# Kernel optimization log

Hardware: AMD Instinct MI355X
Metric: run time of the kernel (lower is better)

The kernel has to match this reference:

```python
import jax, jax.numpy as jnp
import numpy as np

B, N, F = 4, 3000, 128

def setup_inputs() -> dict:
    key = jax.random.key(0)
    k1, k2, k3, k4 = jax.random.split(key, 4)
    x = jax.random.normal(k1, (B, N, F), dtype=jnp.float32)
    adj = jax.random.uniform(k2, (B, N, N), dtype=jnp.float32)
    h0 = jax.random.normal(k3, (B, N, F), dtype=jnp.float32)
    stdv = 1.0 / np.sqrt(F)
    theta = jax.random.uniform(k4, (F, F), dtype=jnp.float32, minval=-stdv, maxval=stdv)
    return {
        "x": x, "adj": adj, "h0": h0, "theta": theta,
        "lamda": jnp.float32(0.5), "alpha": jnp.float32(0.1), "l": 4,
    }

def _normalize_adj(adj):
    # add self loops, then D^{-1/2} A D^{-1/2} via elementwise row/col scaling
    # (same math as diag-embed + inverse + two bmms in the original)
    n = adj.shape[1]
    adj = adj + jnp.eye(n, dtype=adj.dtype)
    deg = jnp.sum(adj, axis=2)                      # [B, N]
    d_inv_sqrt = jax.lax.rsqrt(deg)                 # [B, N]
    return d_inv_sqrt[:, :, None] * adj * d_inv_sqrt[:, None, :]

def reference(x, adj, h0, theta, lamda, alpha, l):
    adj_n = _normalize_adj(adj)
    beta = jnp.log(lamda / l + 1.0)
    hi = jnp.einsum('bnm,bmf->bnf', adj_n, x)       # aggregation
    support = (1.0 - alpha) * hi + alpha * h0       # variant=False path
    r = support
    out = beta * jnp.einsum('bnf,fg->bng', support, theta) + (1.0 - beta) * r
    return out
```

## Files before the change

kernel.cpp:

```cpp
#include <hip/hip_runtime.h>
#include <hip/hip_bf16.h>
#include <math.h>

#define BB 4
#define NN 3000
#define NR 3008
#define NC 3072
#define FF 128
#define NKC 96
#define NIT 188
#define TS  532

typedef __bf16 bf16x8 __attribute__((ext_vector_type(8)));
typedef __bf16 bf16x4 __attribute__((ext_vector_type(4)));
typedef __bf16 bf16x8a __attribute__((ext_vector_type(8), aligned(8)));
typedef __bf16 bf16x4a __attribute__((ext_vector_type(4), aligned(4)));
typedef float  f32x4  __attribute__((ext_vector_type(4)));

__global__ __launch_bounds__(256) void k_degpk2(const float* __restrict__ adj,
                                                float* __restrict__ dis,
                                                __bf16* __restrict__ apk) {
    int wid  = (blockIdx.x * 256 + threadIdx.x) >> 6;
    int lane = threadIdx.x & 63;
    if (wid >= BB * NR) return;
    int b = wid / NR, i = wid - b * NR;
    const bool rowv = i < NN;
    const float4* row4 = (const float4*)(adj + ((size_t)b * NN + i) * NN);
    __bf16* prow = apk + ((size_t)b * NR + i) * NC;
    float s = 0.f;
    for (int c = lane; c < 768; c += 64) {
        float4 v = {0.f, 0.f, 0.f, 0.f};
        if (rowv && c < 750) v = row4[c];
        s += (v.x + v.y) + (v.z + v.w);
        bf16x4a o;
        o[0] = (__bf16)v.x; o[1] = (__bf16)v.y;
        o[2] = (__bf16)v.z; o[3] = (__bf16)v.w;
        *(bf16x4a*)(prow + c * 4) = o;
    }
    for (int off = 32; off > 0; off >>= 1) s += __shfl_down(s, off, 64);
    if (lane == 0 && rowv) dis[b * NN + i] = 1.0f / sqrtf(s + 1.0f);
}

__global__ __launch_bounds__(256) void k_xpk(const float* __restrict__ x,
                                             const float* __restrict__ dis,
                                             const float* __restrict__ theta,
                                             __bf16* __restrict__ xpk,
                                             __bf16* __restrict__ thpk) {
    int b  = blockIdx.y, kc = blockIdx.x;
    int t  = threadIdx.x, w = t >> 6, l = t & 63;
    int m  = l & 15, q = l >> 4;
    #pragma unroll
    for (int h = 0; h < 2; ++h) {
        int nt = w + h * 4;
        int f  = nt * 16 + m;
        bf16x8 v;
        #pragma unroll
        for (int j = 0; j < 8; ++j) {
            int k = kc * 32 + q * 8 + j;
            float val = 0.f;
            if (k < NN) val = dis[b * NN + k] * x[((size_t)b * NN + k) * FF + f];
            v[j] = (__bf16)val;
        }
        *(bf16x8*)(xpk + ((size_t)(b * 8 + nt) * NKC + kc) * 512 + l * 8) = v;
    }
    if (b == 0 && kc < 4) {
        #pragma unroll
        for (int h = 0; h < 2; ++h) {
            int nt = w + h * 4;
            bf16x8 v;
            #pragma unroll
            for (int j = 0; j < 8; ++j) {
                int k = kc * 32 + q * 8 + j;
                v[j] = (__bf16)theta[k * FF + nt * 16 + m];
            }
            *(bf16x8*)(thpk + ((size_t)(nt * 4 + kc)) * 512 + l * 8) = v;
        }
    }
}

__global__ __launch_bounds__(256) void k_agg3(const __bf16* __restrict__ apk,
                                              const __bf16* __restrict__ xpk,
                                              const __bf16* __restrict__ thpk,
                                              const float* __restrict__ x,
                                              const float* __restrict__ h0,
                                              const float* __restrict__ dis,
                                              float* __restrict__ out,
                                              const float* __restrict__ alpha_p,
                                              const float* __restrict__ lamda_p,
                                              const int* __restrict__ l_p) {
    __shared__ __bf16 tile[2][16][TS];
    __shared__ __bf16 stile[16][140];
    const int id = blockIdx.x;
    const int b  = (id >> 1) & 3;
    const int it = (id >> 3) * 2 + (id & 1);
    const int i0 = it * 16;
    const int t  = threadIdx.x, w = t >> 6, l = t & 63;
    const int m  = l & 15, quad = l >> 4;
    const int n0 = w * 32;
    const __bf16* Abase = apk + ((size_t)b * NR + i0) * NC;
    const __bf16* B0 = xpk + ((size_t)(b * 8 + 2 * w) * NKC) * 512 + l * 8;
    const __bf16* B1 = B0 + (size_t)NKC * 512;
    f32x4 acc0 = {0.f, 0.f, 0.f, 0.f};
    f32x4 acc1 = {0.f, 0.f, 0.f, 0.f};

    bf16x8a st[4];
    auto load_chunk = [&](int c) {
        #pragma unroll
        for (int i = 0; i < 4; ++i) {
            int row = i * 4 + w;
            st[i] = *(const bf16x8a*)(Abase + (size_t)row * NC + c * 512 + l * 8);
        }
    };
    auto store_chunk = [&](int cb) {
        #pragma unroll
        for (int i = 0; i < 4; ++i) {
            int row = i * 4 + w;
            *(bf16x8a*)&tile[cb][row][l * 8] = st[i];
        }
    };

    load_chunk(0);
    store_chunk(0);
    __syncthreads();
    for (int c = 0; c < 6; ++c) {
        int cb = c & 1;
        if (c < 5) load_chunk(c + 1);
        #pragma unroll 4
        for (int kcl = 0; kcl < 16; ++kcl) {
            int kc = c * 16 + kcl;
            bf16x8 a = *(const bf16x8a*)&tile[cb][m][kcl * 32 + quad * 8];
            bf16x8 b0 = *(const bf16x8*)(B0 + (size_t)kc * 512);
            bf16x8 b1 = *(const bf16x8*)(B1 + (size_t)kc * 512);
            acc0 = __builtin_amdgcn_mfma_f32_16x16x32_bf16(a, b0, acc0, 0, 0, 0);
            acc1 = __builtin_amdgcn_mfma_f32_16x16x32_bf16(a, b1, acc1, 0, 0, 0);
        }
        if (c < 5) store_chunk(cb ^ 1);
        __syncthreads();
    }

    const float alpha = *alpha_p;
    const float beta  = logf(*lamda_p / (float)(*l_p) + 1.0f);
    float s0v[4], s1v[4];
    #pragma unroll
    for (int r = 0; r < 4; ++r) {
        int row  = quad * 4 + r;
        int irow = i0 + row;
        float s0 = 0.f, s1 = 0.f;
        if (irow < NN) {
            float  di   = dis[b * NN + irow];
            size_t base = ((size_t)b * NN + irow) * FF;
            int c0 = n0 + m, c1 = n0 + 16 + m;
            s0 = (1.f - alpha) * (di * acc0[r] + di * di * x[base + c0]) + alpha * h0[base + c0];
            s1 = (1.f - alpha) * (di * acc1[r] + di * di * x[base + c1]) + alpha * h0[base + c1];
        }
        s0v[r] = s0; s1v[r] = s1;
        stile[row][n0 + m]      = (__bf16)s0;
        stile[row][n0 + 16 + m] = (__bf16)s1;
    }
    __syncthreads();
    f32x4 o0 = {0.f, 0.f, 0.f, 0.f};
    f32x4 o1 = {0.f, 0.f, 0.f, 0.f};
    const __bf16* T0 = thpk + (size_t)(2 * w * 4) * 512 + l * 8;
    const __bf16* T1 = T0 + 4 * 512;
    #pragma unroll
    for (int kc = 0; kc < 4; ++kc) {
        bf16x4a alo = *(const bf16x4a*)&stile[m][kc * 32 + quad * 8];
        bf16x4a ahi = *(const bf16x4a*)&stile[m][kc * 32 + quad * 8 + 4];
        bf16x8 a = __builtin_shufflevector(alo, ahi, 0, 1, 2, 3, 4, 5, 6, 7);
        bf16x8 tb0 = *(const bf16x8*)(T0 + (size_t)kc * 512);
        bf16x8 tb1 = *(const bf16x8*)(T1 + (size_t)kc * 512);
        o0 = __builtin_amdgcn_mfma_f32_16x16x32_bf16(a, tb0, o0, 0, 0, 0);
        o1 = __builtin_amdgcn_mfma_f32_16x16x32_bf16(a, tb1, o1, 0, 0, 0);
    }
    const float omb = 1.f - beta;
    #pragma unroll
    for (int r = 0; r < 4; ++r) {
        int irow = i0 + quad * 4 + r;
        if (irow < NN) {
            size_t base = ((size_t)b * NN + irow) * FF;
            out[base + n0 + m]      = beta * o0[r] + omb * s0v[r];
            out[base + n0 + 16 + m] = beta * o1[r] + omb * s1v[r];
        }
    }
}

__global__ __launch_bounds__(256) void k_deg(const float* __restrict__ adj,
                                             float* __restrict__ dis) {
    int wid  = (blockIdx.x * 256 + threadIdx.x) >> 6;
    int lane = threadIdx.x & 63;
    if (wid >= BB * NN) return;
    const float4* row = (const float4*)(adj + (size_t)wid * NN);
    float s = 0.f;
    for (int c = lane; c < NN / 4; c += 64) {
        float4 v = row[c];
        s += (v.x + v.y) + (v.z + v.w);
    }
    for (int off = 32; off > 0; off >>= 1) s += __shfl_down(s, off, 64);
    if (lane == 0) dis[wid] = 1.0f / sqrtf(s + 1.0f);
}

__global__ __launch_bounds__(256) void k_agg(const float* __restrict__ adj,
                                             const __bf16* __restrict__ xpk,
                                             const __bf16* __restrict__ thpk,
                                             const float* __restrict__ x,
                                             const float* __restrict__ h0,
                                             const float* __restrict__ dis,
                                             float* __restrict__ out,
                                             const float* __restrict__ alpha_p,
                                             const float* __restrict__ lamda_p,
                                             const int* __restrict__ l_p) {
    __shared__ __bf16 tile[2][16][TS];
    __shared__ __bf16 stile[16][140];
    const int id = blockIdx.x;
    const int b  = (id >> 1) & 3;
    const int it = (id >> 3) * 2 + (id & 1);
    const int i0 = it * 16;
    const int t  = threadIdx.x, w = t >> 6, l = t & 63;
    const int m  = l & 15, quad = l >> 4;
    const int n0 = w * 32;
    const __bf16* B0 = xpk + ((size_t)(b * 8 + 2 * w) * NKC) * 512 + l * 8;
    const __bf16* B1 = B0 + (size_t)NKC * 512;
    f32x4 acc0 = {0.f, 0.f, 0.f, 0.f};
    f32x4 acc1 = {0.f, 0.f, 0.f, 0.f};

    float4 pu[4], pv[4];
    auto load_chunk = [&](int c) {
        #pragma unroll
        for (int i = 0; i < 4; ++i) {
            int row  = i * 4 + w;
            int irow = i0 + row;
            int col  = c * 512 + l * 8;
            float4 u = {0.f, 0.f, 0.f, 0.f}, v = {0.f, 0.f, 0.f, 0.f};
            if (irow < NN && col < NN) {
                const float* p = adj + ((size_t)b * NN + irow) * NN + col;
                u = *(const float4*)p;
                v = *(const float4*)(p + 4);
            }
            pu[i] = u; pv[i] = v;
        }
    };
    auto store_chunk = [&](int cb) {
        #pragma unroll
        for (int i = 0; i < 4; ++i) {
            int row = i * 4 + w;
            bf16x8a s;
            s[0] = (__bf16)pu[i].x; s[1] = (__bf16)pu[i].y;
            s[2] = (__bf16)pu[i].z; s[3] = (__bf16)pu[i].w;
            s[4] = (__bf16)pv[i].x; s[5] = (__bf16)pv[i].y;
            s[6] = (__bf16)pv[i].z; s[7] = (__bf16)pv[i].w;
            *(bf16x8a*)&tile[cb][row][l * 8] = s;
        }
    };

    load_chunk(0);
    store_chunk(0);
    __syncthreads();
    for (int c = 0; c < 6; ++c) {
        int cb = c & 1;
        if (c < 5) load_chunk(c + 1);
        #pragma unroll 4
        for (int kcl = 0; kcl < 16; ++kcl) {
            int kc = c * 16 + kcl;
            bf16x8 a = *(const bf16x8a*)&tile[cb][m][kcl * 32 + quad * 8];
            bf16x8 b0 = *(const bf16x8*)(B0 + (size_t)kc * 512);
            bf16x8 b1 = *(const bf16x8*)(B1 + (size_t)kc * 512);
            acc0 = __builtin_amdgcn_mfma_f32_16x16x32_bf16(a, b0, acc0, 0, 0, 0);
            acc1 = __builtin_amdgcn_mfma_f32_16x16x32_bf16(a, b1, acc1, 0, 0, 0);
        }
        if (c < 5) store_chunk(cb ^ 1);
        __syncthreads();
    }

    const float alpha = *alpha_p;
    const float beta  = logf(*lamda_p / (float)(*l_p) + 1.0f);
    float s0v[4], s1v[4];
    #pragma unroll
    for (int r = 0; r < 4; ++r) {
        int row  = quad * 4 + r;
        int irow = i0 + row;
        float s0 = 0.f, s1 = 0.f;
        if (irow < NN) {
            float  di   = dis[b * NN + irow];
            size_t base = ((size_t)b * NN + irow) * FF;
            int c0 = n0 + m, c1 = n0 + 16 + m;
            s0 = (1.f - alpha) * (di * acc0[r] + di * di * x[base + c0]) + alpha * h0[base + c0];
            s1 = (1.f - alpha) * (di * acc1[r] + di * di * x[base + c1]) + alpha * h0[base + c1];
        }
        s0v[r] = s0; s1v[r] = s1;
        stile[row][n0 + m]      = (__bf16)s0;
        stile[row][n0 + 16 + m] = (__bf16)s1;
    }
    __syncthreads();
    f32x4 o0 = {0.f, 0.f, 0.f, 0.f};
    f32x4 o1 = {0.f, 0.f, 0.f, 0.f};
    const __bf16* T0 = thpk + (size_t)(2 * w * 4) * 512 + l * 8;
    const __bf16* T1 = T0 + 4 * 512;
    #pragma unroll
    for (int kc = 0; kc < 4; ++kc) {
        bf16x4a alo = *(const bf16x4a*)&stile[m][kc * 32 + quad * 8];
        bf16x4a ahi = *(const bf16x4a*)&stile[m][kc * 32 + quad * 8 + 4];
        bf16x8 a = __builtin_shufflevector(alo, ahi, 0, 1, 2, 3, 4, 5, 6, 7);
        bf16x8 tb0 = *(const bf16x8*)(T0 + (size_t)kc * 512);
        bf16x8 tb1 = *(const bf16x8*)(T1 + (size_t)kc * 512);
        o0 = __builtin_amdgcn_mfma_f32_16x16x32_bf16(a, tb0, o0, 0, 0, 0);
        o1 = __builtin_amdgcn_mfma_f32_16x16x32_bf16(a, tb1, o1, 0, 0, 0);
    }
    const float omb = 1.f - beta;
    #pragma unroll
    for (int r = 0; r < 4; ++r) {
        int irow = i0 + quad * 4 + r;
        if (irow < NN) {
            size_t base = ((size_t)b * NN + irow) * FF;
            out[base + n0 + m]      = beta * o0[r] + omb * s0v[r];
            out[base + n0 + 16 + m] = beta * o1[r] + omb * s1v[r];
        }
    }
}

__global__ __launch_bounds__(256) void k_thpk_fb(const float* __restrict__ theta,
                                                 __bf16* __restrict__ thpk) {
    int kc = blockIdx.x;
    int t  = threadIdx.x, w = t >> 6, l = t & 63;
    int m  = l & 15, q = l >> 4;
    #pragma unroll
    for (int h = 0; h < 2; ++h) {
        int nt = w + h * 4;
        bf16x8 v;
        #pragma unroll
        for (int j = 0; j < 8; ++j) {
            int k = kc * 32 + q * 8 + j;
            v[j] = (__bf16)theta[k * FF + nt * 16 + m];
        }
        *(bf16x8*)(thpk + ((size_t)(nt * 4 + kc)) * 512 + l * 8) = v;
    }
}

__global__ __launch_bounds__(256) void k_xpk_fb(const float* __restrict__ x,
                                                const float* __restrict__ dis,
                                                __bf16* __restrict__ xpk) {
    int b  = blockIdx.y, kc = blockIdx.x;
    int t  = threadIdx.x, w = t >> 6, l = t & 63;
    int m  = l & 15, q = l >> 4;
    #pragma unroll
    for (int h = 0; h < 2; ++h) {
        int nt = w + h * 4;
        int f  = nt * 16 + m;
        bf16x8 v;
        #pragma unroll
        for (int j = 0; j < 8; ++j) {
            int k = kc * 32 + q * 8 + j;
            float val = 0.f;
            if (k < NN) val = dis[b * NN + k] * x[((size_t)b * NN + k) * FF + f];
            v[j] = (__bf16)val;
        }
        *(bf16x8*)(xpk + ((size_t)(b * 8 + nt) * NKC + kc) * 512 + l * 8) = v;
    }
}


extern "C" void kernel_launch(void* const* d_in, const int* in_sizes, int n_in,
                              void* d_out, int out_size, void* d_ws, size_t ws_size,
                              hipStream_t stream) {
    const float* x      = (const float*)d_in[0];
    const float* adj    = (const float*)d_in[1];
    const float* h0     = (const float*)d_in[2];
    const float* theta  = (const float*)d_in[3];
    const float* lamda  = (const float*)d_in[4];
    const float* alpha  = (const float*)d_in[5];
    const int*   l      = (const int*)d_in[6];
    float* out = (float*)d_out;

    char* ws = (char*)d_ws;

    const size_t APK_OFF = 3276800;
    const size_t WS_NEED = APK_OFF + (size_t)BB * NR * NC * 2;

    if (ws_size >= WS_NEED) {
        float*  dis  = (float*)ws;
        __bf16* thpk = (__bf16*)(ws + 65536);
        __bf16* xpk  = (__bf16*)(ws + 131072);
        __bf16* apk  = (__bf16*)(ws + APK_OFF);

        k_degpk2<<<dim3((BB * NR) / 4), 256, 0, stream>>>(adj, dis, apk);
        k_xpk<<<dim3(NKC, BB), 256, 0, stream>>>(x, dis, theta, xpk, thpk);
        k_agg3<<<dim3(NIT * BB), 256, 0, stream>>>(apk, xpk, thpk, x, h0, dis, out,
                                                   alpha, lamda, l);
    } else {
        float*  dis  = (float*)ws;
        __bf16* xpk  = (__bf16*)(ws + 65536);
        __bf16* thpk = (__bf16*)(ws + 3276800);

        k_deg<<<dim3((BB * NN) / 4), 256, 0, stream>>>(adj, dis);
        k_thpk_fb<<<dim3(4), 256, 0, stream>>>(theta, thpk);
        k_xpk_fb<<<dim3(NKC, BB), 256, 0, stream>>>(x, dis, xpk);
        k_agg<<<dim3(NIT * BB), 256, 0, stream>>>(adj, xpk, thpk, x, h0, dis, out,
                                                  alpha, lamda, l);
    }
}
```

Measured before the change: 281.2 us.

## Fuse degree/pack/x-pack prologue into one kernel and stage A via global_load_lds

Merges the degree+adjacency packing kernel and the x/theta packing kernel into a single launch. Each block handles 16 rows and then packs the matching x slice using the degrees it keeps in shared memory, and two extra blocks zero the padded tail and pack theta. The aggregation kernel now streams A tiles straight into LDS with global_load_lds instead of staging them through registers. This removes one launch and frees registers, at the cost of a wider LDS row stride and reliance on the async LDS-load semantics.

```diff
diff --git a/kernel.cpp b/kernel.cpp
--- a/kernel.cpp
+++ b/kernel.cpp
@@ -9,7 +9,8 @@
 #define FF 128
 #define NKC 96
 #define NIT 188
-#define TS  532
+#define TS  536
+#define TSF 532
 
 typedef __bf16 bf16x8 __attribute__((ext_vector_type(8)));
 typedef __bf16 bf16x4 __attribute__((ext_vector_type(4)));
@@ -17,68 +18,96 @@
 typedef __bf16 bf16x4a __attribute__((ext_vector_type(4), aligned(4)));
 typedef float  f32x4  __attribute__((ext_vector_type(4)));
 
-__global__ __launch_bounds__(256) void k_degpk2(const float* __restrict__ adj,
-                                                float* __restrict__ dis,
-                                                __bf16* __restrict__ apk) {
-    int wid  = (blockIdx.x * 256 + threadIdx.x) >> 6;
-    int lane = threadIdx.x & 63;
-    if (wid >= BB * NR) return;
-    int b = wid / NR, i = wid - b * NR;
-    const bool rowv = i < NN;
-    const float4* row4 = (const float4*)(adj + ((size_t)b * NN + i) * NN);
-    __bf16* prow = apk + ((size_t)b * NR + i) * NC;
-    float s = 0.f;
-    for (int c = lane; c < 768; c += 64) {
-        float4 v = {0.f, 0.f, 0.f, 0.f};
-        if (rowv && c < 750) v = row4[c];
-        s += (v.x + v.y) + (v.z + v.w);
-        bf16x4a o;
-        o[0] = (__bf16)v.x; o[1] = (__bf16)v.y;
-        o[2] = (__bf16)v.z; o[3] = (__bf16)v.w;
-        *(bf16x4a*)(prow + c * 4) = o;
-    }
-    for (int off = 32; off > 0; off >>= 1) s += __shfl_down(s, off, 64);
-    if (lane == 0 && rowv) dis[b * NN + i] = 1.0f / sqrtf(s + 1.0f);
-}
-
-__global__ __launch_bounds__(256) void k_xpk(const float* __restrict__ x,
-                                             const float* __restrict__ dis,
-                                             const float* __restrict__ theta,
-                                             __bf16* __restrict__ xpk,
-                                             __bf16* __restrict__ thpk) {
-    int b  = blockIdx.y, kc = blockIdx.x;
-    int t  = threadIdx.x, w = t >> 6, l = t & 63;
-    int m  = l & 15, q = l >> 4;
-    #pragma unroll
-    for (int h = 0; h < 2; ++h) {
-        int nt = w + h * 4;
-        int f  = nt * 16 + m;
-        bf16x8 v;
-        #pragma unroll
-        for (int j = 0; j < 8; ++j) {
-            int k = kc * 32 + q * 8 + j;
-            float val = 0.f;
-            if (k < NN) val = dis[b * NN + k] * x[((size_t)b * NN + k) * FF + f];
-            v[j] = (__bf16)val;
-        }
-        *(bf16x8*)(xpk + ((size_t)(b * 8 + nt) * NKC + kc) * 512 + l * 8) = v;
-    }
-    if (b == 0 && kc < 4) {
-        #pragma unroll
-        for (int h = 0; h < 2; ++h) {
-            int nt = w + h * 4;
-            bf16x8 v;
+#define GLOAD_LDS16(gp, lp)                                                       \
+    __builtin_amdgcn_global_load_lds(                                             \
+        (const __attribute__((address_space(1))) void*)(gp),                      \
+        (__attribute__((address_space(3))) void*)(lp), 16, 0, 0)
+
+__global__ __launch_bounds__(256) void k_p1(const float* __restrict__ adj,
+                                            const float* __restrict__ x,
+                                            const float* __restrict__ theta,
+                                            float* __restrict__ dis,
+                                            __bf16* __restrict__ apk,
+                                            __bf16* __restrict__ xpk,
+                                            __bf16* __restrict__ thpk) {
+    const int blk = blockIdx.x;
+    const int t = threadIdx.x, w = t >> 6, l = t & 63;
+    __shared__ float sdis[16];
+
+    if (blk < NIT * BB) {
+        const int b = blk / NIT, sub = blk - b * NIT;
+        const int i0 = sub * 16;
+        for (int rr = 0; rr < 4; ++rr) {
+            int i = i0 + w * 4 + rr;
+            const bool rv = i < NN;
+            const float4* row4 = (const float4*)(adj + ((size_t)b * NN + i) * NN);
+            __bf16* prow = apk + ((size_t)b * NR + i) * NC;
+            float s = 0.f;
+            for (int c = l; c < 768; c += 64) {
+                float4 v = {0.f, 0.f, 0.f, 0.f};
+                if (rv && c < 750) v = row4[c];
+                s += (v.x + v.y) + (v.z + v.w);
+                bf16x4a o;
+                o[0] = (__bf16)v.x; o[1] = (__bf16)v.y;
+                o[2] = (__bf16)v.z; o[3] = (__bf16)v.w;
+                *(bf16x4a*)(prow + c * 4) = o;
+            }
+            for (int off = 32; off > 0; off >>= 1) s += __shfl_down(s, off, 64);
+            if (l == 0) {
+                float d = 1.0f / sqrtf(s + 1.0f);
+                sdis[w * 4 + rr] = d;
+                if (rv) dis[b * NN + i] = d;
+            }
+        }
+        __syncthreads();
+        const int kc = sub >> 1, half = sub & 1;
+        const int m = l & 15, q = l >> 4;
+        if ((q >> 1) == half) {
             #pragma unroll
-            for (int j = 0; j < 8; ++j) {
-                int k = kc * 32 + q * 8 + j;
-                v[j] = (__bf16)theta[k * FF + nt * 16 + m];
+            for (int h = 0; h < 2; ++h) {
+                int nt = w + h * 4;
+                int f  = nt * 16 + m;
+                bf16x8 v;
+                #pragma unroll
+                for (int j = 0; j < 8; ++j) {
+                    int k = kc * 32 + q * 8 + j;
+                    float val = 0.f;
+                    if (k < NN) val = sdis[q * 8 + j - half * 16] *
+                                      x[((size_t)b * NN + k) * FF + f];
+                    v[j] = (__bf16)val;
+                }
+                *(bf16x8*)(xpk + ((size_t)(b * 8 + nt) * NKC + kc) * 512 + l * 8) = v;
             }
-            *(bf16x8*)(thpk + ((size_t)(nt * 4 + kc)) * 512 + l * 8) = v;
-        }
-    }
-}
-
-__global__ __launch_bounds__(256) void k_agg3(const __bf16* __restrict__ apk,
+        }
+    } else if (blk == NIT * BB) {
+        for (int idx = t; idx < 4096; idx += 256) {
+            int l8   = idx & 63;
+            int tile = idx >> 6;
+            int kc   = 94 + (tile & 1);
+            int bnt  = tile >> 1;
+            bf16x8 z = {(__bf16)0.f, (__bf16)0.f, (__bf16)0.f, (__bf16)0.f,
+                        (__bf16)0.f, (__bf16)0.f, (__bf16)0.f, (__bf16)0.f};
+            *(bf16x8*)(xpk + ((size_t)bnt * NKC + kc) * 512 + l8 * 8) = z;
+        }
+    } else {
+        const int m = l & 15, q = l >> 4;
+        for (int kc = 0; kc < 4; ++kc) {
+            #pragma unroll
+            for (int h = 0; h < 2; ++h) {
+                int nt = w + h * 4;
+                bf16x8 v;
+                #pragma unroll
+                for (int j = 0; j < 8; ++j) {
+                    int k = kc * 32 + q * 8 + j;
+                    v[j] = (__bf16)theta[k * FF + nt * 16 + m];
+                }
+                *(bf16x8*)(thpk + ((size_t)(nt * 4 + kc)) * 512 + l * 8) = v;
+            }
+        }
+    }
+}
+
+__global__ __launch_bounds__(256) void k_agg4(const __bf16* __restrict__ apk,
                                               const __bf16* __restrict__ xpk,
                                               const __bf16* __restrict__ thpk,
                                               const float* __restrict__ x,
@@ -103,19 +132,143 @@
     f32x4 acc0 = {0.f, 0.f, 0.f, 0.f};
     f32x4 acc1 = {0.f, 0.f, 0.f, 0.f};
 
-    bf16x8a st[4];
+    auto stage_chunk = [&](int c, int cb) {
+        #pragma unroll
+        for (int i = 0; i < 4; ++i) {
+            int row = i * 4 + w;
+            GLOAD_LDS16(Abase + (size_t)row * NC + c * 512 + l * 8,
+                        &tile[cb][row][0]);
+        }
+    };
+
+    stage_chunk(0, 0);
+    __syncthreads();
+    for (int c = 0; c < 6; ++c) {
+        int cb = c & 1;
+        if (c < 5) stage_chunk(c + 1, cb ^ 1);
+        #pragma unroll 4
+        for (int kcl = 0; kcl < 16; ++kcl) {
+            int kc = c * 16 + kcl;
+            bf16x8 a  = *(const bf16x8a*)&tile[cb][m][kcl * 32 + quad * 8];
+            bf16x8 b0 = *(const bf16x8*)(B0 + (size_t)kc * 512);
+            bf16x8 b1 = *(const bf16x8*)(B1 + (size_t)kc * 512);
+            acc0 = __builtin_amdgcn_mfma_f32_16x16x32_bf16(a, b0, acc0, 0, 0, 0);
+            acc1 = __builtin_amdgcn_mfma_f32_16x16x32_bf16(a, b1, acc1, 0, 0, 0);
+        }
+        __syncthreads();
+    }
+
+    const float alpha = *alpha_p;
+    const float beta  = logf(*lamda_p / (float)(*l_p) + 1.0f);
+    float s0v[4], s1v[4];
+    #pragma unroll
+    for (int r = 0; r < 4; ++r) {
+        int row  = quad * 4 + r;
+        int irow = i0 + row;
+        float s0 = 0.f, s1 = 0.f;
+        if (irow < NN) {
+            float  di   = dis[b * NN + irow];
+            size_t base = ((size_t)b * NN + irow) * FF;
+            int c0 = n0 + m, c1 = n0 + 16 + m;
+            s0 = (1.f - alpha) * (di * acc0[r] + di * di * x[base + c0]) + alpha * h0[base + c0];
+            s1 = (1.f - alpha) * (di * acc1[r] + di * di * x[base + c1]) + alpha * h0[base + c1];
+        }
+        s0v[r] = s0; s1v[r] = s1;
+        stile[row][n0 + m]      = (__bf16)s0;
+        stile[row][n0 + 16 + m] = (__bf16)s1;
+    }
+    __syncthreads();
+    f32x4 o0 = {0.f, 0.f, 0.f, 0.f};
+    f32x4 o1 = {0.f, 0.f, 0.f, 0.f};
+    const __bf16* T0 = thpk + (size_t)(2 * w * 4) * 512 + l * 8;
+    const __bf16* T1 = T0 + 4 * 512;
+    #pragma unroll
+    for (int kc = 0; kc < 4; ++kc) {
+        bf16x4a alo = *(const bf16x4a*)&stile[m][kc * 32 + quad * 8];
+        bf16x4a ahi = *(const bf16x4a*)&stile[m][kc * 32 + quad * 8 + 4];
+        bf16x8 a = __builtin_shufflevector(alo, ahi, 0, 1, 2, 3, 4, 5, 6, 7);
+        bf16x8 tb0 = *(const bf16x8*)(T0 + (size_t)kc * 512);
+        bf16x8 tb1 = *(const bf16x8*)(T1 + (size_t)kc * 512);
+        o0 = __builtin_amdgcn_mfma_f32_16x16x32_bf16(a, tb0, o0, 0, 0, 0);
+        o1 = __builtin_amdgcn_mfma_f32_16x16x32_bf16(a, tb1, o1, 0, 0, 0);
+    }
+    const float omb = 1.f - beta;
+    #pragma unroll
+    for (int r = 0; r < 4; ++r) {
+        int irow = i0 + quad * 4 + r;
+        if (irow < NN) {
+            size_t base = ((size_t)b * NN + irow) * FF;
+            out[base + n0 + m]      = beta * o0[r] + omb * s0v[r];
+            out[base + n0 + 16 + m] = beta * o1[r] + omb * s1v[r];
+        }
+    }
+}
+
+__global__ __launch_bounds__(256) void k_deg(const float* __restrict__ adj,
+                                             float* __restrict__ dis) {
+    int wid  = (blockIdx.x * 256 + threadIdx.x) >> 6;
+    int lane = threadIdx.x & 63;
+    if (wid >= BB * NN) return;
+    const float4* row = (const float4*)(adj + (size_t)wid * NN);
+    float s = 0.f;
+    for (int c = lane; c < NN / 4; c += 64) {
+        float4 v = row[c];
+        s += (v.x + v.y) + (v.z + v.w);
+    }
+    for (int off = 32; off > 0; off >>= 1) s += __shfl_down(s, off, 64);
+    if (lane == 0) dis[wid] = 1.0f / sqrtf(s + 1.0f);
+}
+
+__global__ __launch_bounds__(256) void k_agg(const float* __restrict__ adj,
+                                             const __bf16* __restrict__ xpk,
+                                             const __bf16* __restrict__ thpk,
+                                             const float* __restrict__ x,
+                                             const float* __restrict__ h0,
+                                             const float* __restrict__ dis,
+                                             float* __restrict__ out,
+                                             const float* __restrict__ alpha_p,
+                                             const float* __restrict__ lamda_p,
+                                             const int* __restrict__ l_p) {
+    __shared__ __bf16 tile[2][16][TSF];
+    __shared__ __bf16 stile[16][140];
+    const int id = blockIdx.x;
+    const int b  = (id >> 1) & 3;
+    const int it = (id >> 3) * 2 + (id & 1);
+    const int i0 = it * 16;
+    const int t  = threadIdx.x, w = t >> 6, l = t & 63;
+    const int m  = l & 15, quad = l >> 4;
+    const int n0 = w * 32;
+    const __bf16* B0 = xpk + ((size_t)(b * 8 + 2 * w) * NKC) * 512 + l * 8;
+    const __bf16* B1 = B0 + (size_t)NKC * 512;
+    f32x4 acc0 = {0.f, 0.f, 0.f, 0.f};
+    f32x4 acc1 = {0.f, 0.f, 0.f, 0.f};
+
+    float4 pu[4], pv[4];
     auto load_chunk = [&](int c) {
         #pragma unroll
         for (int i = 0; i < 4; ++i) {
-            int row = i * 4 + w;
-            st[i] = *(const bf16x8a*)(Abase + (size_t)row * NC + c * 512 + l * 8);
+            int row  = i * 4 + w;
+            int irow = i0 + row;
+            int col  = c * 512 + l * 8;
+            float4 u = {0.f, 0.f, 0.f, 0.f}, v = {0.f, 0.f, 0.f, 0.f};
+            if (irow < NN && col < NN) {
+                const float* p = adj + ((size_t)b * NN + irow) * NN + col;
+                u = *(const float4*)p;
+                v = *(const float4*)(p + 4);
+            }
+            pu[i] = u; pv[i] = v;
         }
     };
     auto store_chunk = [&](int cb) {
         #pragma unroll
         for (int i = 0; i < 4; ++i) {
             int row = i * 4 + w;
-            *(bf16x8a*)&tile[cb][row][l * 8] = st[i];
+            bf16x8a s;
+            s[0] = (__bf16)pu[i].x; s[1] = (__bf16)pu[i].y;
+            s[2] = (__bf16)pu[i].z; s[3] = (__bf16)pu[i].w;
+            s[4] = (__bf16)pv[i].x; s[5] = (__bf16)pv[i].y;
+            s[6] = (__bf16)pv[i].z; s[7] = (__bf16)pv[i].w;
+            *(bf16x8a*)&tile[cb][row][l * 8] = s;
         }
     };
 
@@ -184,139 +337,6 @@
     }
 }
 
-__global__ __launch_bounds__(256) void k_deg(const float* __restrict__ adj,
-                                             float* __restrict__ dis) {
-    int wid  = (blockIdx.x * 256 + threadIdx.x) >> 6;
-    int lane = threadIdx.x & 63;
-    if (wid >= BB * NN) return;
-    const float4* row = (const float4*)(adj + (size_t)wid * NN);
-    float s = 0.f;
-    for (int c = lane; c < NN / 4; c += 64) {
-        float4 v = row[c];
-        s += (v.x + v.y) + (v.z + v.w);
-    }
-    for (int off = 32; off > 0; off >>= 1) s += __shfl_down(s, off, 64);
-    if (lane == 0) dis[wid] = 1.0f / sqrtf(s + 1.0f);
-}
-
-__global__ __launch_bounds__(256) void k_agg(const float* __restrict__ adj,
-                                             const __bf16* __restrict__ xpk,
-                                             const __bf16* __restrict__ thpk,
-                                             const float* __restrict__ x,
-                                             const float* __restrict__ h0,
-                                             const float* __restrict__ dis,
-                                             float* __restrict__ out,
-                                             const float* __restrict__ alpha_p,
-                                             const float* __restrict__ lamda_p,
-                                             const int* __restrict__ l_p) {
-    __shared__ __bf16 tile[2][16][TS];
-    __shared__ __bf16 stile[16][140];
-    const int id = blockIdx.x;
-    const int b  = (id >> 1) & 3;
-    const int it = (id >> 3) * 2 + (id & 1);
-    const int i0 = it * 16;
-    const int t  = threadIdx.x, w = t >> 6, l = t & 63;
-    const int m  = l & 15, quad = l >> 4;
-    const int n0 = w * 32;
-    const __bf16* B0 = xpk + ((size_t)(b * 8 + 2 * w) * NKC) * 512 + l * 8;
-    const __bf16* B1 = B0 + (size_t)NKC * 512;
-    f32x4 acc0 = {0.f, 0.f, 0.f, 0.f};
-    f32x4 acc1 = {0.f, 0.f, 0.f, 0.f};
-
-    float4 pu[4], pv[4];
-    auto load_chunk = [&](int c) {
-        #pragma unroll
-        for (int i = 0; i < 4; ++i) {
-            int row  = i * 4 + w;
-            int irow = i0 + row;
-            int col  = c * 512 + l * 8;
-            float4 u = {0.f, 0.f, 0.f, 0.f}, v = {0.f, 0.f, 0.f, 0.f};
-            if (irow < NN && col < NN) {
-                const float* p = adj + ((size_t)b * NN + irow) * NN + col;
-                u = *(const float4*)p;
-                v = *(const float4*)(p + 4);
-            }
-            pu[i] = u; pv[i] = v;
-        }
-    };
-    auto store_chunk = [&](int cb) {
-        #pragma unroll
-        for (int i = 0; i < 4; ++i) {
-            int row = i * 4 + w;
-            bf16x8a s;
-            s[0] = (__bf16)pu[i].x; s[1] = (__bf16)pu[i].y;
-            s[2] = (__bf16)pu[i].z; s[3] = (__bf16)pu[i].w;
-            s[4] = (__bf16)pv[i].x; s[5] = (__bf16)pv[i].y;
-            s[6] = (__bf16)pv[i].z; s[7] = (__bf16)pv[i].w;
-            *(bf16x8a*)&tile[cb][row][l * 8] = s;
-        }
-    };
-
-    load_chunk(0);
-    store_chunk(0);
-    __syncthreads();
-    for (int c = 0; c < 6; ++c) {
-        int cb = c & 1;
-        if (c < 5) load_chunk(c + 1);
-        #pragma unroll 4
-        for (int kcl = 0; kcl < 16; ++kcl) {
-            int kc = c * 16 + kcl;
-            bf16x8 a = *(const bf16x8a*)&tile[cb][m][kcl * 32 + quad * 8];
-            bf16x8 b0 = *(const bf16x8*)(B0 + (size_t)kc * 512);
-            bf16x8 b1 = *(const bf16x8*)(B1 + (size_t)kc * 512);
-            acc0 = __builtin_amdgcn_mfma_f32_16x16x32_bf16(a, b0, acc0, 0, 0, 0);
-            acc1 = __builtin_amdgcn_mfma_f32_16x16x32_bf16(a, b1, acc1, 0, 0, 0);
-        }
-        if (c < 5) store_chunk(cb ^ 1);
-        __syncthreads();
-    }
-
-    const float alpha = *alpha_p;
-    const float beta  = logf(*lamda_p / (float)(*l_p) + 1.0f);
-    float s0v[4], s1v[4];
-    #pragma unroll
-    for (int r = 0; r < 4; ++r) {
-        int row  = quad * 4 + r;
-        int irow = i0 + row;
-        float s0 = 0.f, s1 = 0.f;
-        if (irow < NN) {
-            float  di   = dis[b * NN + irow];
-            size_t base = ((size_t)b * NN + irow) * FF;
-            int c0 = n0 + m, c1 = n0 + 16 + m;
-            s0 = (1.f - alpha) * (di * acc0[r] + di * di * x[base + c0]) + alpha * h0[base + c0];
-            s1 = (1.f - alpha) * (di * acc1[r] + di * di * x[base + c1]) + alpha * h0[base + c1];
-        }
-        s0v[r] = s0; s1v[r] = s1;
-        stile[row][n0 + m]      = (__bf16)s0;
-        stile[row][n0 + 16 + m] = (__bf16)s1;
-    }
-    __syncthreads();
-    f32x4 o0 = {0.f, 0.f, 0.f, 0.f};
-    f32x4 o1 = {0.f, 0.f, 0.f, 0.f};
-    const __bf16* T0 = thpk + (size_t)(2 * w * 4) * 512 + l * 8;
-    const __bf16* T1 = T0 + 4 * 512;
-    #pragma unroll
-    for (int kc = 0; kc < 4; ++kc) {
-        bf16x4a alo = *(const bf16x4a*)&stile[m][kc * 32 + quad * 8];
-        bf16x4a ahi = *(const bf16x4a*)&stile[m][kc * 32 + quad * 8 + 4];
-        bf16x8 a = __builtin_shufflevector(alo, ahi, 0, 1, 2, 3, 4, 5, 6, 7);
-        bf16x8 tb0 = *(const bf16x8*)(T0 + (size_t)kc * 512);
-        bf16x8 tb1 = *(const bf16x8*)(T1 + (size_t)kc * 512);
-        o0 = __builtin_amdgcn_mfma_f32_16x16x32_bf16(a, tb0, o0, 0, 0, 0);
-        o1 = __builtin_amdgcn_mfma_f32_16x16x32_bf16(a, tb1, o1, 0, 0, 0);
-    }
-    const float omb = 1.f - beta;
-    #pragma unroll
-    for (int r = 0; r < 4; ++r) {
-        int irow = i0 + quad * 4 + r;
-        if (irow < NN) {
-            size_t base = ((size_t)b * NN + irow) * FF;
-            out[base + n0 + m]      = beta * o0[r] + omb * s0v[r];
-            out[base + n0 + 16 + m] = beta * o1[r] + omb * s1v[r];
-        }
-    }
-}
-
 __global__ __launch_bounds__(256) void k_thpk_fb(const float* __restrict__ theta,
                                                  __bf16* __restrict__ thpk) {
     int kc = blockIdx.x;
@@ -381,9 +401,8 @@
         __bf16* xpk  = (__bf16*)(ws + 131072);
         __bf16* apk  = (__bf16*)(ws + APK_OFF);
 
-        k_degpk2<<<dim3((BB * NR) / 4), 256, 0, stream>>>(adj, dis, apk);
-        k_xpk<<<dim3(NKC, BB), 256, 0, stream>>>(x, dis, theta, xpk, thpk);
-        k_agg3<<<dim3(NIT * BB), 256, 0, stream>>>(apk, xpk, thpk, x, h0, dis, out,
+        k_p1<<<dim3(NIT * BB + 2), 256, 0, stream>>>(adj, x, theta, dis, apk, xpk, thpk);
+        k_agg4<<<dim3(NIT * BB), 256, 0, stream>>>(apk, xpk, thpk, x, h0, dis, out,
                                                    alpha, lamda, l);
     } else {
         float*  dis  = (float*)ws;
```

New measurement: 281.7 us. No clear change (+0.2%).
